# Optimization experiments

Hardware: AMD Instinct MI355X
Metric: run time of the kernel (lower is better)

## Reference

```python
import jax, jax.numpy as jnp
import numpy as np

NUM_HEADS = 8
WINDOW = 33  # must be odd for seq length to be preserved


def setup_inputs() -> dict:
    key = jax.random.key(0)
    ks = jax.random.split(key, 7)
    B, S, E = 4, 2048, 256
    sc = 1.0 / np.sqrt(E)
    return {
        "x": jax.random.normal(ks[0], (B, S, E), dtype=jnp.float32),
        "Wq": jax.random.normal(ks[1], (E, E), dtype=jnp.float32) * sc,
        "bq": jax.random.normal(ks[2], (E,), dtype=jnp.float32) * 0.01,
        "Wk": jax.random.normal(ks[3], (E, E), dtype=jnp.float32) * sc,
        "bk": jax.random.normal(ks[4], (E,), dtype=jnp.float32) * 0.01,
        "Wv": jax.random.normal(ks[5], (E, E), dtype=jnp.float32) * sc,
        "bv": jax.random.normal(ks[6], (E,), dtype=jnp.float32) * 0.01,
    }


def reference(x, Wq, bq, Wk, bk, Wv, bv):
    B, S, E = x.shape
    H = NUM_HEADS
    D = E // H
    W = WINDOW
    pad = (W - 1) // 2
    scale = D ** (-0.5)

    def heads(t):  # [B,S,E] -> [B,H,S,D]
        return t.reshape(B, S, H, D).transpose(0, 2, 1, 3)

    q = heads(x @ Wq + bq)
    k = heads(x @ Wk + bk)
    v = heads(x @ Wv + bv)

    K = S - W + 1  # number of k/v windows (unfold with step=1)
    kv_idx = jnp.arange(K)[:, None] + jnp.arange(W)[None, :]  # [K,W]
    k_unf = k[:, :, kv_idx, :]  # [B,H,K,W,D]
    v_unf = v[:, :, kv_idx, :]  # [B,H,K,W,D]

    q_pad = jnp.pad(q, ((0, 0), (0, 0), (pad, pad), (0, 0)))  # zero pad seq
    q_idx = jnp.arange(S)[:, None] + jnp.arange(W)[None, :]  # [S,W]
    q_unf = q_pad[:, :, q_idx, :]  # [B,H,S,W,D]

    # contract over BOTH window and head dim (faithful to the torch einsums)
    scores = jnp.einsum('bhqwd,bhkwd->bhqk', q_unf, k_unf) * scale  # [B,H,S,K]
    attn = jax.nn.softmax(scores, axis=-1)
    out = jnp.einsum('bhqk,bhkwd->bhqd', attn, v_unf)  # sums v over window too
    return out.transpose(0, 2, 1, 3).reshape(B, S, E)
```

## Files before the change

kernel.cpp:

```cpp
#include <hip/hip_runtime.h>
#include <hip/hip_bf16.h>
#include <math.h>

#define BB   4
#define SS   2048
#define EE   256
#define HH   8
#define DD   32
#define WW   33
#define KKN  (SS - WW + 1)
#define SCALE 0.17677669529663687f
#define FMAX 20.0f
#define SCALE2 0.25503486f
#define FM2    28.853900817779268f

typedef __attribute__((ext_vector_type(8))) short short8v;
typedef __attribute__((ext_vector_type(4))) short short4v;
typedef __attribute__((ext_vector_type(4))) float float4v;

__device__ __forceinline__ short f2bf(float f) {
    union { __hip_bfloat16 h; short s; } c;
    c.h = __float2bfloat16(f);
    return c.s;
}

__device__ __forceinline__ float bf2f(short h) {
    union { unsigned u; float f; } c;
    c.u = ((unsigned)(unsigned short)h) << 16;
    return c.f;
}

__device__ __forceinline__ short2 f2bf2(float a, float b) {
    union { __hip_bfloat162 h; short2 s; } c;
    float2 f; f.x = a; f.y = b;
    c.h = __float22bfloat162_rn(f);
    return c.s;
}

#if __has_builtin(__builtin_amdgcn_exp2f)
__device__ __forceinline__ float exp2_fast(float x) { return __builtin_amdgcn_exp2f(x); }
#else
__device__ __forceinline__ float exp2_fast(float x) { return __expf(x * 0.6931471805599453f); }
#endif

__global__ __launch_bounds__(256) void cvt_kernel(
    const float* __restrict__ Wq, const float* __restrict__ Wk,
    const float* __restrict__ Wv,
    short* __restrict__ wth, short* __restrict__ wtl)
{
    const int t  = threadIdx.x;
    const int bx = blockIdx.x;
    int o   = bx * 2048 + t * 8;
    int mat = o >> 16;
    int rem = o & 65535;
    int n = rem >> 8, k0 = rem & 255;
    const float* W = (mat == 0) ? Wq : (mat == 1) ? Wk : Wv;
    short8v h, l;
#pragma unroll
    for (int j = 0; j < 8; j++) {
        float f = W[(size_t)(k0 + j) * 256 + n];
        short hb = f2bf(f);
        h[j] = hb;
        l[j] = f2bf(f - bf2f(hb));
    }
    *(short8v*)(wth + o) = h;
    *(short8v*)(wtl + o) = l;
}

__global__ __launch_bounds__(256) void proj_kernel(
    const float* __restrict__ x,
    const short* __restrict__ wth, const short* __restrict__ wtl,
    const float* __restrict__ bq, const float* __restrict__ bk,
    const float* __restrict__ bv,
    short* __restrict__ qo, short* __restrict__ ko, float* __restrict__ vo)
{
    __shared__ alignas(16) short xsh[64][40];
    __shared__ alignas(16) short xsl[64][40];
    __shared__ alignas(16) short wsh[128][40];
    __shared__ alignas(16) short wsl[128][40];

    const int t   = threadIdx.x;
    const int r0  = blockIdx.x * 64;
    const int mat = blockIdx.y >> 1;
    const int cb  = blockIdx.y & 1;
    const int lane = t & 63, wv = t >> 6;
    const int quad = lane >> 4, lr = lane & 15;
    const float* bias = (mat == 0) ? bq : (mat == 1) ? bk : bv;
    const size_t wofs = (size_t)(mat * 256 + cb * 128) * 256;
    const short* wthm = wth + wofs;
    const short* wtlm = wtl + wofs;

    float4v acc[8];
#pragma unroll
    for (int ct = 0; ct < 8; ct++) acc[ct] = (float4v){0.f, 0.f, 0.f, 0.f};

    for (int kk = 0; kk < 8; kk++) {
        __syncthreads();
        {
            int r = t >> 2, c8 = (t & 3) * 8;
            const float* xp = x + (size_t)(r0 + r) * 256 + kk * 32 + c8;
            float4 f0 = *(const float4*)xp;
            float4 f1 = *(const float4*)(xp + 4);
            float f[8] = {f0.x, f0.y, f0.z, f0.w, f1.x, f1.y, f1.z, f1.w};
            short8v h, l;
#pragma unroll
            for (int j = 0; j < 8; j++) {
                short hb = f2bf(f[j]);
                h[j] = hb;
                l[j] = f2bf(f[j] - bf2f(hb));
            }
            *(short8v*)&xsh[r][c8] = h;
            *(short8v*)&xsl[r][c8] = l;
        }
#pragma unroll
        for (int i = 0; i < 2; i++) {
            int L = t + i * 256;
            int wr = L >> 2, c8 = (L & 3) * 8;
            size_t go = (size_t)wr * 256 + kk * 32 + c8;
            *(short8v*)&wsh[wr][c8] = *(const short8v*)(wthm + go);
            *(short8v*)&wsl[wr][c8] = *(const short8v*)(wtlm + go);
        }
        __syncthreads();

        const short8v ah = *(const short8v*)&xsh[wv * 16 + lr][quad * 8];
        const short8v al = *(const short8v*)&xsl[wv * 16 + lr][quad * 8];
#pragma unroll
        for (int ct = 0; ct < 8; ct++) {
            const short8v bh_ = *(const short8v*)&wsh[ct * 16 + lr][quad * 8];
            const short8v bl_ = *(const short8v*)&wsl[ct * 16 + lr][quad * 8];
            acc[ct] = __builtin_amdgcn_mfma_f32_16x16x32_bf16(ah, bh_, acc[ct], 0, 0, 0);
            acc[ct] = __builtin_amdgcn_mfma_f32_16x16x32_bf16(ah, bl_, acc[ct], 0, 0, 0);
            acc[ct] = __builtin_amdgcn_mfma_f32_16x16x32_bf16(al, bh_, acc[ct], 0, 0, 0);
        }
    }

    short* op = (mat == 0) ? qo : ko;
#pragma unroll
    for (int ct = 0; ct < 8; ct++) {
        int col = cb * 128 + ct * 16 + lr;
        float bv_ = bias[col];
        int h = col >> 5, d = col & 31;
#pragma unroll
        for (int e = 0; e < 4; e++) {
            int row = r0 + wv * 16 + quad * 4 + e;
            int b_ = row >> 11, s = row & 2047;
            size_t o = (((size_t)(b_ * HH + h)) * SS + s) * DD + d;
            if (mat == 2) vo[o] = acc[ct][e] + bv_;
            else          op[o] = f2bf(acc[ct][e] + bv_);
        }
    }
}

__global__ __launch_bounds__(64) void vs_kernel(
    const float* __restrict__ v, short* __restrict__ vsT)
{
    const int t   = threadIdx.x;
    const int d4  = t & 7;
    const int kkb = blockIdx.x * 8 + (t >> 3);
    const int bh  = blockIdx.y;
    if (kkb >= 252) return;
    const int kb0 = kkb * 8;

    const float4* vp = (const float4*)(v + ((size_t)bh * SS + kb0) * DD) + d4;
    float4 rbuf[7];
    float4 acc = {0.f, 0.f, 0.f, 0.f};
#pragma unroll
    for (int w = 0; w < WW; w++) {
        float4 xv = vp[w * 8];
        if (w < 7) rbuf[w] = xv;
        acc.x += xv.x; acc.y += xv.y; acc.z += xv.z; acc.w += xv.w;
    }
    short8v sh[4];
    sh[0][0] = f2bf(acc.x); sh[1][0] = f2bf(acc.y);
    sh[2][0] = f2bf(acc.z); sh[3][0] = f2bf(acc.w);
#pragma unroll
    for (int s = 1; s < 8; s++) {
        float4 sub = rbuf[s - 1];
        float4 add = vp[(s + 32) * 8];
        acc.x += add.x - sub.x; acc.y += add.y - sub.y;
        acc.z += add.z - sub.z; acc.w += add.w - sub.w;
        sh[0][s] = f2bf(acc.x); sh[1][s] = f2bf(acc.y);
        sh[2][s] = f2bf(acc.z); sh[3][s] = f2bf(acc.w);
    }
#pragma unroll
    for (int j = 0; j < 4; j++) {
        short* op = vsT + ((size_t)bh * DD + 4 * d4 + j) * KKN + kb0;
        *(short8v*)op = sh[j];
    }
}

__global__ __launch_bounds__(256, 4) void attn_kernel(
    const short* __restrict__ qg, const short* __restrict__ kg,
    const short* __restrict__ vsTg, float* __restrict__ out)
{
    __shared__ alignas(16) short QbS[64][40];
    __shared__ alignas(16) short Kb[96][40];
    __shared__ alignas(16) short Gst[96][72];
    __shared__ alignas(16) short vT[32][72];
    __shared__ float lrow[32];

    short (*Qb)[40] = QbS;
    short (*pb)[72] = (short (*)[72])QbS;

    const int t  = threadIdx.x;
    const int qt = blockIdx.x;
    const int bh = blockIdx.y;
    const int q0 = qt * 32;

    const short* qb   = qg   + (size_t)bh * SS * DD;
    const short* kb   = kg   + (size_t)bh * SS * DD;
    const short* vsTb = vsTg + (size_t)bh * DD * KKN;

    const int lane = t & 63, wv = t >> 6;
    const int quad = lane >> 4, lr = lane & 15;
    const int ptm = wv >> 1, ptn = wv & 1;
    const int jcol = 64 + (t & 7);

    const int qitw  = wv & 1;
    const int tbase = wv >> 1;
    const int qi    = qitw * 16 + lr;

    const int vd  = t >> 3, vc8 = (t & 7) * 8;
    const int r2  = t >> 2, c8r = (t & 3) * 8;

    {
        short8v z = {0, 0, 0, 0, 0, 0, 0, 0};
        short* g = &Gst[0][0];
        for (int i = t; i < 864; i += 256) *(short8v*)(g + 8 * i) = z;
    }

    {
        int gq = q0 - 16 + r2;
        if (gq >= 0 && gq < SS) {
            *(short8v*)&Qb[r2][c8r] = *(const short8v*)(qb + (size_t)gq * DD + c8r);
        } else {
            float4 z = {0.f, 0.f, 0.f, 0.f};
            *(float4*)&Qb[r2][c8r] = z;
        }
        *(short8v*)&Kb[r2][c8r] = *(const short8v*)(kb + (size_t)r2 * DD + c8r);
        if (t < 128)
            *(short8v*)&Kb[64 + r2][c8r] = *(const short8v*)(kb + (size_t)(64 + r2) * DD + c8r);
    }
    if (t < 32) lrow[t] = 0.f;
    __syncthreads();

    short8v Qf[4];
#pragma unroll
    for (int tq = 0; tq < 4; tq++)
        Qf[tq] = *(const short8v*)&Qb[tq * 16 + lr][quad * 8];

    short8v Ufw[2];
#pragma unroll
    for (int ch = 0; ch < 2; ch++) {
        short8v u;
#pragma unroll
        for (int j = 0; j < 8; j++) {
            int m = ch * 32 + quad * 8 + j;
            u[j] = (qi <= m && m <= qi + 32) ? (short)0x3F80 : (short)0;
        }
        Ufw[ch] = u;
    }

    float4v acc = {0.f, 0.f, 0.f, 0.f};
    float lsumw = 0.f;
    const int npass = (wv < 2) ? 2 : 1;
    int k0m = 0;

    for (int kt = 0; kt < 32; kt++) {
        const int k0 = kt * 64;
        for (int pass = 0; pass < npass; pass++) {
            const int tk = wv + pass * 4;
            int krow = k0m + tk * 16 + lr; if (krow >= 96) krow -= 96;
            const short8v A = *(const short8v*)&Kb[krow][quad * 8];
#pragma unroll
            for (int tq = 0; tq < 4; tq++) {
                const int del = tk - tq;
                if (del < -2 || del > 4) continue;
                float4v c0 = {0.f, 0.f, 0.f, 0.f};
                c0 = __builtin_amdgcn_mfma_f32_16x16x32_bf16(A, Qf[tq], c0, 0, 0, 0);
                const int i   = tq * 16 + lr;
                const int j2b = tk * 16 + quad * 4 - i + 31;
                short* gbase = &Gst[0][i];
                short2 g01 = f2bf2(c0[0], c0[1]);
                short2 g23 = f2bf2(c0[2], c0[3]);
                short gv[4] = {g01.x, g01.y, g23.x, g23.y};
#pragma unroll
                for (int e = 0; e < 4; e++) {
                    int j2 = j2b + e;
                    short* dst = ((unsigned)j2 < 95u) ? (gbase + j2 * 72)
                                                      : (gbase + 95 * 72);
                    *dst = gv[e];
                }
            }
        }

        if (kt > 0) {
            const short8v Ap0 = *(const short8v*)&pb[ptm * 16 + lr][quad * 8];
            const short8v Ap1 = *(const short8v*)&pb[ptm * 16 + lr][32 + quad * 8];
            const short8v Bv0 = *(const short8v*)&vT[ptn * 16 + lr][quad * 8];
            const short8v Bv1 = *(const short8v*)&vT[ptn * 16 + lr][32 + quad * 8];
            __builtin_amdgcn_s_setprio(1);
            acc = __builtin_amdgcn_mfma_f32_16x16x32_bf16(Ap0, Bv0, acc, 0, 0, 0);
            acc = __builtin_amdgcn_mfma_f32_16x16x32_bf16(Ap1, Bv1, acc, 0, 0, 0);
            __builtin_amdgcn_s_setprio(0);
        }
        __syncthreads();

        {
            int col = k0 + vc8; if (col > KKN - 8) col = KKN - 8;
            *(short8v*)&vT[vd][vc8] = *(const short8v*)(vsTb + (size_t)vd * KKN + col);
        }
        if (kt < 31) {
            int gp = k0 + 96 + r2;
            int ga = (gp < SS) ? gp : (SS - 1);
            int slot = k0m + r2; if (slot >= 96) slot -= 96;
            *(short8v*)&Kb[slot][c8r] = *(const short8v*)(kb + (size_t)ga * DD + c8r);
        }

        const unsigned lim = (kt == 31) ? 32u : 64u;
        if (kt == 31) {
            short4v z4 = {0, 0, 0, 0};
            int zr = t >> 3, zc = (t & 7) * 4 + 32;
            *(short4v*)&pb[zr][zc] = z4;
        }

        short* prow = &pb[qi][0];
#pragma unroll
        for (int u = 0; u < 3; u++) {
            const int tile = 2 * u + tbase;
            const int jrow = tile * 16 + lr;
            const short8v A0f = *(const short8v*)&Gst[jrow][quad * 8];
            const short8v A1f = *(const short8v*)&Gst[jrow][32 + quad * 8];
            float4v D = {0.f, 0.f, 0.f, 0.f};
            __builtin_amdgcn_s_setprio(1);
            D = __builtin_amdgcn_mfma_f32_16x16x32_bf16(A0f, Ufw[0], D, 0, 0, 0);
            D = __builtin_amdgcn_mfma_f32_16x16x32_bf16(A1f, Ufw[1], D, 0, 0, 0);
            __builtin_amdgcn_s_setprio(0);
            const int kib = qi + tile * 16 + quad * 4 - 31;
            float p0 = exp2_fast(fmaf(D[0], SCALE2, -FM2));
            float p1 = exp2_fast(fmaf(D[1], SCALE2, -FM2));
            float p2 = exp2_fast(fmaf(D[2], SCALE2, -FM2));
            float p3 = exp2_fast(fmaf(D[3], SCALE2, -FM2));
            short2 c01 = f2bf2(p0, p1);
            short2 c23 = f2bf2(p2, p3);
            float pv[4] = {p0, p1, p2, p3};
            short cv[4] = {c01.x, c01.y, c23.x, c23.y};
#pragma unroll
            for (int e = 0; e < 4; e++) {
                int ki = kib + e;
                bool ok = (unsigned)ki < lim;
                short* dst = ok ? (prow + ki) : (prow + jcol);
                *dst = cv[e];
                lsumw += ok ? pv[e] : 0.f;
            }
        }
        __syncthreads();
        k0m += 64; if (k0m >= 96) k0m -= 96;
    }

    {
        const short8v Ap0 = *(const short8v*)&pb[ptm * 16 + lr][quad * 8];
        const short8v Ap1 = *(const short8v*)&pb[ptm * 16 + lr][32 + quad * 8];
        const short8v Bv0 = *(const short8v*)&vT[ptn * 16 + lr][quad * 8];
        const short8v Bv1 = *(const short8v*)&vT[ptn * 16 + lr][32 + quad * 8];
        acc = __builtin_amdgcn_mfma_f32_16x16x32_bf16(Ap0, Bv0, acc, 0, 0, 0);
        acc = __builtin_amdgcn_mfma_f32_16x16x32_bf16(Ap1, Bv1, acc, 0, 0, 0);
    }

    {
        float s = lsumw;
        s += __shfl_xor(s, 16);
        s += __shfl_xor(s, 32);
        if (quad == 0) atomicAdd(&lrow[qitw * 16 + lr], s);
    }
    __syncthreads();

    {
        const int rrow = ptm * 16 + quad * 4;
        const int col  = ptn * 16 + lr;
        const int b_ = bh >> 3, h = bh & 7;
#pragma unroll
        for (int e = 0; e < 4; e++) {
            int s_ = q0 + rrow + e;
            out[((size_t)(b_ * SS + s_)) * EE + h * DD + col] = acc[e] / lrow[rrow + e];
        }
    }
}

extern "C" void kernel_launch(void* const* d_in, const int* in_sizes, int n_in,
                              void* d_out, int out_size, void* d_ws, size_t ws_size,
                              hipStream_t stream)
{
    (void)in_sizes; (void)n_in; (void)out_size; (void)ws_size;
    const float* x  = (const float*)d_in[0];
    const float* Wq = (const float*)d_in[1];
    const float* bq = (const float*)d_in[2];
    const float* Wk = (const float*)d_in[3];
    const float* bk = (const float*)d_in[4];
    const float* Wv = (const float*)d_in[5];
    const float* bv = (const float*)d_in[6];
    float* out = (float*)d_out;

    const size_t REG = (size_t)BB * HH * SS * DD;
    short* qbf   = (short*)d_ws;
    short* kbf   = qbf + REG;
    float* vbuf  = (float*)(kbf + REG);
    short* vsTb  = (short*)(vbuf + REG);

    short* wth = (short*)out;
    short* wtl = wth + 3 * 256 * 256;

    cvt_kernel<<<dim3(96), dim3(256), 0, stream>>>(Wq, Wk, Wv, wth, wtl);
    proj_kernel<<<dim3(128, 6), dim3(256), 0, stream>>>(x, wth, wtl,
                                                        bq, bk, bv,
                                                        qbf, kbf, vbuf);
    vs_kernel<<<dim3(32, 32), dim3(64), 0, stream>>>(vbuf, vsTb);
    attn_kernel<<<dim3(64, 32), dim3(256), 0, stream>>>(qbf, kbf, vsTb, out);
}
```

Before: 249.7 us.

## Prefetch K/V tiles into registers early and rebalance score MFMA work across waves

Global loads for the next V and K tiles are issued at the top of each iteration into registers and written to shared memory after the barrier, so their latency overlaps the score MFMAs. The second score pass, previously done only by waves 0-1, is now spread across all four waves, with each wave handling a subset of q tiles for k tiles 4-5. Launch bounds drop from 4 to 3 blocks per SM to leave room for the extra live registers, which may reduce occupancy.

```diff
diff --git a/kernel.cpp b/kernel.cpp
--- a/kernel.cpp
+++ b/kernel.cpp
@@ -189,7 +189,7 @@
     }
 }
 
-__global__ __launch_bounds__(256, 4) void attn_kernel(
+__global__ __launch_bounds__(256, 3) void attn_kernel(
     const short* __restrict__ qg, const short* __restrict__ kg,
     const short* __restrict__ vsTg, float* __restrict__ out)
 {
@@ -223,6 +223,10 @@
     const int vd  = t >> 3, vc8 = (t & 7) * 8;
     const int r2  = t >> 2, c8r = (t & 3) * 8;
 
+    const int tk2   = 4 + (wv & 1);
+    const int t2lo  = (wv >> 1) * 2 + (wv & 1);
+    const int t2hi  = (wv == 3) ? 3 : (t2lo + 1);
+
     {
         short8v z = {0, 0, 0, 0, 0, 0, 0, 0};
         short* g = &Gst[0][0];
@@ -263,13 +267,24 @@
 
     float4v acc = {0.f, 0.f, 0.f, 0.f};
     float lsumw = 0.f;
-    const int npass = (wv < 2) ? 2 : 1;
     int k0m = 0;
 
     for (int kt = 0; kt < 32; kt++) {
         const int k0 = kt * 64;
-        for (int pass = 0; pass < npass; pass++) {
-            const int tk = wv + pass * 4;
+        short8v vstage;
+        {
+            int col = k0 + vc8; if (col > KKN - 8) col = KKN - 8;
+            vstage = *(const short8v*)(vsTb + (size_t)vd * KKN + col);
+        }
+        short8v kstage;
+        if (kt < 31) {
+            int gp = k0 + 96 + r2;
+            int ga = (gp < SS) ? gp : (SS - 1);
+            kstage = *(const short8v*)(kb + (size_t)ga * DD + c8r);
+        }
+
+        {
+            const int tk = wv;
             int krow = k0m + tk * 16 + lr; if (krow >= 96) krow -= 96;
             const short8v A = *(const short8v*)&Kb[krow][quad * 8];
 #pragma unroll
@@ -293,6 +308,30 @@
                 }
             }
         }
+        {
+            const int tk = tk2;
+            int krow = k0m + tk * 16 + lr; if (krow >= 96) krow -= 96;
+            const short8v A = *(const short8v*)&Kb[krow][quad * 8];
+#pragma unroll
+            for (int tq = 0; tq < 4; tq++) {
+                if (tq < t2lo || tq > t2hi) continue;
+                float4v c0 = {0.f, 0.f, 0.f, 0.f};
+                c0 = __builtin_amdgcn_mfma_f32_16x16x32_bf16(A, Qf[tq], c0, 0, 0, 0);
+                const int i   = tq * 16 + lr;
+                const int j2b = tk * 16 + quad * 4 - i + 31;
+                short* gbase = &Gst[0][i];
+                short2 g01 = f2bf2(c0[0], c0[1]);
+                short2 g23 = f2bf2(c0[2], c0[3]);
+                short gv[4] = {g01.x, g01.y, g23.x, g23.y};
+#pragma unroll
+                for (int e = 0; e < 4; e++) {
+                    int j2 = j2b + e;
+                    short* dst = ((unsigned)j2 < 95u) ? (gbase + j2 * 72)
+                                                      : (gbase + 95 * 72);
+                    *dst = gv[e];
+                }
+            }
+        }
 
         if (kt > 0) {
             const short8v Ap0 = *(const short8v*)&pb[ptm * 16 + lr][quad * 8];
@@ -306,15 +345,10 @@
         }
         __syncthreads();
 
-        {
-            int col = k0 + vc8; if (col > KKN - 8) col = KKN - 8;
-            *(short8v*)&vT[vd][vc8] = *(const short8v*)(vsTb + (size_t)vd * KKN + col);
-        }
+        *(short8v*)&vT[vd][vc8] = vstage;
         if (kt < 31) {
-            int gp = k0 + 96 + r2;
-            int ga = (gp < SS) ? gp : (SS - 1);
             int slot = k0m + r2; if (slot >= 96) slot -= 96;
-            *(short8v*)&Kb[slot][c8r] = *(const short8v*)(kb + (size_t)ga * DD + c8r);
+            *(short8v*)&Kb[slot][c8r] = kstage;
         }
 
         const unsigned lim = (kt == 31) ? 32u : 64u;
```

Measured after the change: 246.4 us. Within noise of the previous version (-1.3%).
